# Kernel optimization log

Measured on AMD Instinct MI355X. Metric: run time of the kernel, lower is better.

The kernel has to match this reference:

```python
import jax, jax.numpy as jnp
import numpy as np

N_USERS = 100000
N_TWEETS = 100000
N_NODES = N_USERS + N_TWEETS
N_EDGES = 600000
D = 128


def lrelu(x):
    return jax.nn.leaky_relu(x, negative_slope=0.01)


def linear(x, W, b):
    # torch nn.Linear convention: W is [out, in]
    return x @ W.T + b


def rgcn_conv(x, edge_index, edge_type, weight, root, bias):
    """PyG RGCNConv with num_relations=2, aggr='mean', root weight + bias."""
    src, dst = edge_index[0], edge_index[1]
    m = x[src]  # [E, D] gathered source features
    out = x @ root + bias
    for r in range(weight.shape[0]):
        mask = (edge_type == r).astype(x.dtype)  # [E]
        s = jax.ops.segment_sum(m * mask[:, None], dst, num_segments=N_NODES)
        cnt = jax.ops.segment_sum(mask, dst, num_segments=N_NODES)
        mean = s / jnp.maximum(cnt, 1.0)[:, None]  # nodes w/o rel-r in-edges -> 0
        out = out + mean @ weight[r]
    return out


def setup_inputs() -> dict:
    key = jax.random.key(0)
    ks = jax.random.split(key, 24)

    def lin(k, out_d, in_d):
        k1, k2 = jax.random.split(k)
        s = 1.0 / np.sqrt(in_d)
        return (jax.random.uniform(k1, (out_d, in_d), jnp.float32, -s, s),
                jax.random.uniform(k2, (out_d,), jnp.float32, -s, s))

    des = jax.random.normal(ks[0], (N_USERS, 100), jnp.float32)
    tweet = jax.random.normal(ks[1], (N_TWEETS, 100), jnp.float32)
    num_prop = jax.random.normal(ks[2], (N_USERS, 6), jnp.float32)
    cat_prop = jax.random.normal(ks[3], (N_USERS, 11), jnp.float32)
    edge_index = jax.random.randint(ks[4], (2, N_EDGES), 0, N_NODES, jnp.int32)
    edge_type = jax.random.randint(ks[5], (N_EDGES,), 0, 2, jnp.int32)

    W_des, b_des = lin(ks[6], D // 2, 100)       # des -> 64
    W_num, b_num = lin(ks[7], D // 4, 6)         # num_prop -> 32
    W_cat, b_cat = lin(ks[8], D // 4, 11)        # cat_prop -> 32
    W_tw, b_tw = lin(ks[9], D, 100)              # tweet -> 128
    W_in, b_in = lin(ks[10], D, D)
    rgcn_w = jax.random.normal(ks[11], (2, D, D), jnp.float32) / np.sqrt(D)
    rgcn_root = jax.random.normal(ks[12], (D, D), jnp.float32) / np.sqrt(D)
    rgcn_bias = jnp.zeros((D,), jnp.float32)
    W_o1, b_o1 = lin(ks[13], D, D)
    W_o2, b_o2 = lin(ks[14], 2, D)

    return dict(des=des, tweet=tweet, num_prop=num_prop, cat_prop=cat_prop,
                edge_index=edge_index, edge_type=edge_type,
                W_des=W_des, b_des=b_des, W_num=W_num, b_num=b_num,
                W_cat=W_cat, b_cat=b_cat, W_tw=W_tw, b_tw=b_tw,
                W_in=W_in, b_in=b_in, rgcn_w=rgcn_w, rgcn_root=rgcn_root,
                rgcn_bias=rgcn_bias, W_o1=W_o1, b_o1=b_o1, W_o2=W_o2, b_o2=b_o2)


def reference(des, tweet, num_prop, cat_prop, edge_index, edge_type,
              W_des, b_des, W_num, b_num, W_cat, b_cat, W_tw, b_tw,
              W_in, b_in, rgcn_w, rgcn_root, rgcn_bias, W_o1, b_o1, W_o2, b_o2):
    d = lrelu(linear(des, W_des, b_des))
    n = lrelu(linear(num_prop, W_num, b_num))
    c = lrelu(linear(cat_prop, W_cat, b_cat))
    x_users = jnp.concatenate([d, n, c], axis=1)       # [N_users, 128]
    t = lrelu(linear(tweet, W_tw, b_tw))               # [N_tweets, 128]
    x = jnp.concatenate([x_users, t], axis=0)          # [N_nodes, 128]
    x = lrelu(linear(x, W_in, b_in))
    x = rgcn_conv(x, edge_index, edge_type, rgcn_w, rgcn_root, rgcn_bias)
    # dropout in eval mode = identity
    x = rgcn_conv(x, edge_index, edge_type, rgcn_w, rgcn_root, rgcn_bias)
    x = lrelu(linear(x, W_o1, b_o1))
    return linear(x, W_o2, b_o2)
```

## Files before the change

kernel.cpp:

```cpp
#include <hip/hip_runtime.h>
#include <hip/hip_bf16.h>

typedef __hip_bfloat16 bf16;

typedef __bf16 bfv8 __attribute__((ext_vector_type(8)));
typedef float f32x4 __attribute__((ext_vector_type(4)));

__device__ __forceinline__ float lrelu(float x) { return x > 0.f ? x : 0.01f * x; }

__device__ __forceinline__ float ldv(float v) { return v; }
__device__ __forceinline__ float ldv(bf16 v) { return __bfloat162float(v); }
__device__ __forceinline__ void stv(float* p, float v) { *p = v; }
__device__ __forceinline__ void stv(bf16* p, float v) { *p = __float2bfloat16(v); }

__device__ __forceinline__ float in_rd(const void* p, size_t i, int isbf) {
  return isbf ? __bfloat162float(((const bf16*)p)[i]) : ((const float*)p)[i];
}
__device__ __forceinline__ int ix_rd(const void* p, size_t i, int is64) {
  return is64 ? (int)((const long long*)p)[i] : ((const int*)p)[i];
}

struct ProbeArgs {
  const void* p[23];
  int s[23];
  int mode[23];
};

__global__ void detect_all(ProbeArgs a, int* __restrict__ flags) {
  __shared__ int sh[256];
  int b = blockIdx.x;
  const unsigned int* w = (const unsigned int*)a.p[b];
  int s = a.s[b], mode = a.mode[b];
  int t = threadIdx.x;
  int c = 0;
  if (t < s) {
    if (mode == 0) {
      unsigned int v = w[t];
      int e = (v >> 7) & 0xFF;
      c = (e >= 100 && e <= 140) ? 1 : 0;
    } else {
      c = (w[2 * t + 1] == 0u) ? 1 : 0;
    }
  }
  sh[t] = c;
  __syncthreads();
  for (int d = 128; d; d >>= 1) {
    if (t < d) sh[t] += sh[t + d];
    __syncthreads();
  }
  if (t == 0) flags[b] = (mode == 0) ? (sh[0] * 10 >= 7 * s) : (sh[0] * 10 >= 9 * s);
}

#define PW_F32 82562
#define BF_BASE 82564
#define PW_W_TOTAL (BF_BASE + 5 * 8192)
#define ENC_BASE PW_W_TOTAL
#define PW_TOTAL (ENC_BASE + 16384 + 256)
__global__ void prep_weights(const void* Win, const void* bin, const void* rw,
                             const void* root, const void* rb, const void* Wo1,
                             const void* bo1, const void* Wo2, const void* bo2,
                             const int* __restrict__ fl, float* __restrict__ pw) {
  int i = blockIdx.x * 256 + threadIdx.x;
  if (i >= PW_W_TOTAL) return;
  if (i < 16384) {
    int k = i >> 7, o = i & 127;
    pw[i] = in_rd(Win, (size_t)o * 128 + k, fl[14]);
  } else if (i < 32768) {
    int j = i - 16384;
    int k = j >> 7, o = j & 127;
    pw[i] = in_rd(Wo1, (size_t)o * 128 + k, fl[19]);
  } else if (i < 49152) {
    pw[i] = in_rd(root, i - 32768, fl[17]);
  } else if (i < 81920) {
    pw[i] = in_rd(rw, i - 49152, fl[16]);
  } else if (i < 82048) {
    pw[i] = in_rd(bin, i - 81920, fl[15]);
  } else if (i < 82176) {
    pw[i] = in_rd(rb, i - 82048, fl[18]);
  } else if (i < 82304) {
    pw[i] = in_rd(bo1, i - 82176, fl[20]);
  } else if (i < 82560) {
    pw[i] = in_rd(Wo2, i - 82304, fl[21]);
  } else if (i < PW_F32) {
    pw[i] = in_rd(bo2, i - 82560, fl[22]);
  } else if (i >= BF_BASE) {
    int j = i - BF_BASE;
    bf16* bw = (bf16*)(pw + BF_BASE);
#pragma unroll
    for (int q = 0; q < 2; q++) {
      int u = 2 * j + q;
      int m = u >> 14, r = u & 16383;
      int n = r >> 7, k = r & 127;
      float v;
      if (m == 0) v = in_rd(Win, (size_t)n * 128 + k, fl[14]);
      else if (m == 1) v = in_rd(Wo1, (size_t)n * 128 + k, fl[19]);
      else if (m == 2) v = in_rd(root, (size_t)k * 128 + n, fl[17]);
      else v = in_rd(rw, (size_t)(m - 3) * 16384 + (size_t)k * 128 + n, fl[16]);
      bw[u] = __float2bfloat16(v);
    }
  }
}

__global__ void prep_enc(const void* Wd, const void* bd, const void* Wn, const void* bn,
                         const void* Wc, const void* bc, const void* Wt, const void* bt,
                         const int* __restrict__ fl, int dDes, int dNum, int dCat, int dTw,
                         float* __restrict__ pw) {
  int i = blockIdx.x * 256 + threadIdx.x;
  bf16* e = (bf16*)(pw + ENC_BASE);
  float* bU = pw + ENC_BASE + 16384;
  float* bT = bU + 128;
  if (i < 16384) {
    int n = i >> 7, k = i & 127;
    float v = 0.f;
    if (n < 64) {
      if (k < dDes) v = in_rd(Wd, (size_t)n * dDes + k, fl[6]);
    } else if (n < 96) {
      int kk = k - dDes;
      if (kk >= 0 && kk < dNum) v = in_rd(Wn, (size_t)(n - 64) * dNum + kk, fl[8]);
    } else {
      int kk = k - dDes - dNum;
      if (kk >= 0 && kk < dCat) v = in_rd(Wc, (size_t)(n - 96) * dCat + kk, fl[10]);
    }
    e[i] = __float2bfloat16(v);
  } else if (i < 32768) {
    int j = i - 16384;
    int n = j >> 7, k = j & 127;
    float v = (k < dTw) ? in_rd(Wt, (size_t)n * dTw + k, fl[12]) : 0.f;
    e[i] = __float2bfloat16(v);
  } else if (i < 32896) {
    int j = i - 32768;
    bU[j] = (j < 64) ? in_rd(bd, j, fl[7])
                     : (j < 96) ? in_rd(bn, j - 64, fl[9]) : in_rd(bc, j - 96, fl[11]);
  } else if (i < 33024) {
    bT[i - 32896] = in_rd(bt, i - 32896, fl[13]);
  }
}

__global__ void sig_fill(float* __restrict__ p, int n, float v) {
  int i = blockIdx.x * 256 + threadIdx.x;
  if (i < n) p[i] = v;
}
__global__ void zero_ints(int* __restrict__ p, int n) {
  int i = blockIdx.x * 256 + threadIdx.x;
  if (i < n) p[i] = 0;
}

__global__ void count_edges(const void* __restrict__ ei, const void* __restrict__ et,
                            const int* __restrict__ fl, int* __restrict__ cnt, int NEr,
                            int NNr) {
  int e = blockIdx.x * 256 + threadIdx.x;
  if (e >= NEr) return;
  int d = ix_rd(ei, (size_t)NEr + e, fl[4]);
  int r = ix_rd(et, e, fl[5]) & 1;
  if ((unsigned)d >= (unsigned)NNr) return;
  atomicAdd(&cnt[r * NNr + d], 1);
}

__global__ void scan_blocks(const int* __restrict__ in, int* __restrict__ out,
                            int* __restrict__ bsum, int n) {
  __shared__ int sh[256];
  int t = threadIdx.x;
  int base = blockIdx.x * 1024 + t * 4;
  int a[4];
  int s = 0;
#pragma unroll
  for (int i = 0; i < 4; i++) {
    a[i] = (base + i < n) ? in[base + i] : 0;
    s += a[i];
  }
  sh[t] = s;
  __syncthreads();
  for (int d = 1; d < 256; d <<= 1) {
    int v = (t >= d) ? sh[t - d] : 0;
    __syncthreads();
    sh[t] += v;
    __syncthreads();
  }
  int ex = sh[t] - s;
#pragma unroll
  for (int i = 0; i < 4; i++) {
    if (base + i < n) out[base + i] = ex;
    ex += a[i];
  }
  if (t == 255 && bsum) bsum[blockIdx.x] = sh[255];
}

__global__ void scan_add_inv(int* __restrict__ off, const int* __restrict__ bsumsc,
                             const int* __restrict__ cnt, float* __restrict__ inv, int n) {
  int i = blockIdx.x * 256 + threadIdx.x;
  if (i >= n) return;
  off[i] += bsumsc[i >> 10];
  inv[i] = 1.f / fmaxf((float)cnt[i], 1.f);
}

__global__ void fill_elist(const void* __restrict__ ei, const void* __restrict__ et,
                           const int* __restrict__ fl, const int* __restrict__ off,
                           int* __restrict__ fill, int* __restrict__ elist, int NEr, int NNr) {
  int e = blockIdx.x * 256 + threadIdx.x;
  if (e >= NEr) return;
  int s = ix_rd(ei, e, fl[4]);
  int d = ix_rd(ei, (size_t)NEr + e, fl[4]);
  int r = ix_rd(et, e, fl[5]) & 1;
  if ((unsigned)d >= (unsigned)NNr || (unsigned)s >= (unsigned)NNr) return;
  int idx = r * NNr + d;
  int slot = off[idx] + atomicAdd(&fill[idx], 1);
  elist[slot] = s | ((d & 127) << 24);
}

__global__ __launch_bounds__(256) void enc_gemm(const void* __restrict__ A,
                                                const void* __restrict__ W,
                                                const void* __restrict__ B,
                                                const int* __restrict__ fl, int fa, int fw,
                                                int fb, bf16* __restrict__ x, int M, int K,
                                                int N, int row0, int col0) {
  __shared__ float Wb[128 * 102];
  __shared__ float bb[128];
  int t = threadIdx.x;
  int stride = (K & 1) ? K : K + 1;
  int fA = fl[fa];
  {
    int fW = fl[fw], fB = fl[fb];
    for (int idx = t; idx < N * K; idx += 256) {
      int j = idx / K, k = idx - j * K;
      Wb[j * stride + k] = in_rd(W, (size_t)j * K + k, fW);
    }
    if (t < N) bb[t] = in_rd(B, t, fB);
  }
  __syncthreads();
  int j = t % N;
  int r = t / N;
  int R = 256 / N;
  int iEnd = blockIdx.x * 64 + 64;
  if (iEnd > M) iEnd = M;
  const float* wrow = &Wb[j * stride];
  if (!fA) {
    const float* Af = (const float*)A;
    for (int i = blockIdx.x * 64 + r; i < iEnd; i += R) {
      const float* a = Af + (size_t)i * K;
      float acc = bb[j];
      for (int k = 0; k < K; k++) acc += a[k] * wrow[k];
      stv(&x[(size_t)(row0 + i) * 128 + col0 + j], lrelu(acc));
    }
  } else {
    const bf16* Ab = (const bf16*)A;
    for (int i = blockIdx.x * 64 + r; i < iEnd; i += R) {
      const bf16* a = Ab + (size_t)i * K;
      float acc = bb[j];
      for (int k = 0; k < K; k++) acc += __bfloat162float(a[k]) * wrow[k];
      stv(&x[(size_t)(row0 + i) * 128 + col0 + j], lrelu(acc));
    }
  }
}


__global__ __launch_bounds__(256) void enc_mfma(
    const void* __restrict__ A0, const void* __restrict__ A1, const void* __restrict__ A2,
    const int* __restrict__ fl, int fi0, int fi1, int fi2, int K0, int K1, int K2,
    const bf16* __restrict__ WbE, const float* __restrict__ biasE,
    const bf16* __restrict__ WbL, const float* __restrict__ bL, bf16* __restrict__ x,
    int M, int row0) {
  __shared__ __align__(16) bf16 Xs[16384];
  int t = threadIdx.x;
  int i0 = blockIdx.x * 128;

  {
    uint4 z = {0u, 0u, 0u, 0u};
#pragma unroll
    for (int i = 0; i < 8; i++) *(uint4*)((char*)Xs + i * 4096 + t * 16) = z;
  }
  __syncthreads();

  const void* As[3] = {A0, A1, A2};
  int Ks_[3] = {K0, K1, K2};
  int fis[3] = {fi0, fi1, fi2};
  int cb = 0;
  for (int s = 0; s < 3; s++) {
    int Ks = Ks_[s];
    if (Ks <= 0) continue;
    int isbf = fl[fis[s]];
    const void* A = As[s];
    int total = 128 * Ks;
    for (int f = t; f < total; f += 256) {
      int row = f / Ks;
      int k = f - row * Ks;
      int gr = i0 + row;
      float v = (gr < M) ? in_rd(A, (size_t)gr * Ks + k, isbf) : 0.f;
      int byte = row * 256 + (cb + k) * 2;
      *(bf16*)((char*)Xs + (byte ^ ((row & 7) << 4))) = __float2bfloat16(v);
    }
    cb += Ks;
  }
  __syncthreads();

  int wv = t >> 6, l = t & 63;
  int lr = l & 15, lg = l >> 4;
  int rbase = (wv >> 1) * 64, cbase = (wv & 1) * 64;
  int ko = lg * 8;
  f32x4 acc[4][4] = {};
#pragma unroll
  for (int ks = 0; ks < 4; ks++) {
    bfv8 bk[4];
#pragma unroll
    for (int cg = 0; cg < 4; cg++)
      bk[cg] = *(const bfv8*)&WbE[(size_t)(cbase + cg * 16 + lr) * 128 + ks * 32 + ko];
    bfv8 af[4];
#pragma unroll
    for (int rg = 0; rg < 4; rg++) {
      int mrow = rbase + rg * 16 + lr;
      int byte = mrow * 256 + (ks * 32 + ko) * 2;
      af[rg] = *(const bfv8*)((const char*)Xs + (byte ^ ((mrow & 7) << 4)));
    }
#pragma unroll
    for (int rg = 0; rg < 4; rg++)
#pragma unroll
      for (int cg = 0; cg < 4; cg++)
        acc[rg][cg] =
            __builtin_amdgcn_mfma_f32_16x16x32_bf16(af[rg], bk[cg], acc[rg][cg], 0, 0, 0);
  }
  __syncthreads();

#pragma unroll
  for (int cg = 0; cg < 4; cg++) {
    int col = cbase + cg * 16 + lr;
    float bv = biasE[col];
#pragma unroll
    for (int rg = 0; rg < 4; rg++) {
      int r0 = rbase + rg * 16 + lg * 4;
#pragma unroll
      for (int j = 0; j < 4; j++) {
        int row = r0 + j;
        int byte = row * 256 + col * 2;
        *(bf16*)((char*)Xs + (byte ^ ((row & 7) << 4))) =
            __float2bfloat16(lrelu(acc[rg][cg][j] + bv));
      }
    }
  }
  __syncthreads();

  f32x4 acc2[4][4] = {};
#pragma unroll
  for (int ks = 0; ks < 4; ks++) {
    bfv8 bk[4];
#pragma unroll
    for (int cg = 0; cg < 4; cg++)
      bk[cg] = *(const bfv8*)&WbL[(size_t)(cbase + cg * 16 + lr) * 128 + ks * 32 + ko];
    bfv8 af[4];
#pragma unroll
    for (int rg = 0; rg < 4; rg++) {
      int mrow = rbase + rg * 16 + lr;
      int byte = mrow * 256 + (ks * 32 + ko) * 2;
      af[rg] = *(const bfv8*)((const char*)Xs + (byte ^ ((mrow & 7) << 4)));
    }
#pragma unroll
    for (int rg = 0; rg < 4; rg++)
#pragma unroll
      for (int cg = 0; cg < 4; cg++)
        acc2[rg][cg] =
            __builtin_amdgcn_mfma_f32_16x16x32_bf16(af[rg], bk[cg], acc2[rg][cg], 0, 0, 0);
  }

#pragma unroll
  for (int cg = 0; cg < 4; cg++) {
    int col = cbase + cg * 16 + lr;
    float bv = bL[col];
#pragma unroll
    for (int rg = 0; rg < 4; rg++) {
      int r0 = i0 + rbase + rg * 16 + lg * 4;
#pragma unroll
      for (int j = 0; j < 4; j++) {
        int row = r0 + j;
        if (row < M)
          x[(size_t)(row0 + row) * 128 + col] = __float2bfloat16(lrelu(acc2[rg][cg][j] + bv));
      }
    }
  }
}

__global__ __launch_bounds__(256) void mfma_lin(const bf16* __restrict__ A,
                                                const bf16* __restrict__ Wb,
                                                const float* __restrict__ bias,
                                                bf16* __restrict__ Out, int M) {
  int t = threadIdx.x;
  int wv = t >> 6, l = t & 63;
  int lr = l & 15, lg = l >> 4;
  int i0 = blockIdx.x * 128;
  int rbase = (wv >> 1) * 64;
  int cbase = (wv & 1) * 64;
  int ko = lg * 8;

  size_t rowoff[4];
#pragma unroll
  for (int rg = 0; rg < 4; rg++) {
    int row = i0 + rbase + rg * 16 + lr;
    if (row > M - 1) row = M - 1;
    rowoff[rg] = (size_t)row * 128;
  }

  bfv8 bfr[4][4];
#pragma unroll
  for (int cg = 0; cg < 4; cg++)
#pragma unroll
    for (int ks = 0; ks < 4; ks++)
      bfr[cg][ks] = *(const bfv8*)&Wb[(size_t)(cbase + cg * 16 + lr) * 128 + ks * 32 + ko];

  f32x4 acc[4][4] = {};
#pragma unroll
  for (int ks = 0; ks < 4; ks++) {
    bfv8 af[4];
#pragma unroll
    for (int rg = 0; rg < 4; rg++) af[rg] = *(const bfv8*)&A[rowoff[rg] + ks * 32 + ko];
#pragma unroll
    for (int rg = 0; rg < 4; rg++)
#pragma unroll
      for (int cg = 0; cg < 4; cg++)
        acc[rg][cg] =
            __builtin_amdgcn_mfma_f32_16x16x32_bf16(af[rg], bfr[cg][ks], acc[rg][cg], 0, 0, 0);
  }

#pragma unroll
  for (int cg = 0; cg < 4; cg++) {
    int col = cbase + cg * 16 + lr;
    float bv = bias[col];
#pragma unroll
    for (int rg = 0; rg < 4; rg++) {
      int row0 = i0 + rbase + rg * 16 + lg * 4;
#pragma unroll
      for (int j = 0; j < 4; j++) {
        int row = row0 + j;
        if (row < M) Out[(size_t)row * 128 + col] = __float2bfloat16(lrelu(acc[rg][cg][j] + bv));
      }
    }
  }
}

template <bool TAIL>
__global__ __launch_bounds__(256, 4) void mfma_conv_f(
    const bf16* __restrict__ X, const int* __restrict__ off, const int* __restrict__ cnt,
    const int* __restrict__ elist, const float* __restrict__ inv,
    const bf16* __restrict__ WB, const float* __restrict__ bias, bf16* __restrict__ Out,
    const bf16* __restrict__ Wo1B, const float* __restrict__ bO1,
    const float* __restrict__ Wo2, const float* __restrict__ bo2,
    float* __restrict__ out2, int M, int NNr, int NEr) {
  __shared__ __align__(16) float At[64 * 128];
  int t = threadIdx.x;
  int wv = t >> 6, l = t & 63;
  int lr = l & 15, lg = l >> 4;
  int i0 = blockIdx.x * 32;
  int cbase = wv * 32;
  int ko = lg * 8;

  {
    int c8 = (t & 15) * 8;
    int stc[4], dgc[4];
#pragma unroll
    for (int pn = 0; pn < 4; pn++) {
      int vr = (t >> 4) + pn * 16;
      int rel = vr >> 5, m = vr & 31;
      int node = i0 + m;
      int idx = rel * NNr + node;
      bool ok = node < M;
      stc[pn] = ok ? off[idx] : 0;
      dgc[pn] = ok ? cnt[idx] : 0;
    }
    int dmax = max(max(dgc[0], dgc[1]), max(dgc[2], dgc[3]));
    float s[4][8] = {};

    auto xoff = [&](int pn, int e) -> size_t {
      int ec = e < dgc[pn] - 1 ? e : dgc[pn] - 1;
      ec = ec < 0 ? 0 : ec;
      int ei = stc[pn] + ec;
      ei = ei < NEr - 1 ? ei : NEr - 1;
      return (size_t)(elist[ei] & 0xFFFFFF) * 128 + c8;
    };

    bfv8 v0[4], v1[4];
#pragma unroll
    for (int pn = 0; pn < 4; pn++) v0[pn] = *(const bfv8*)&X[xoff(pn, 0)];
#pragma unroll
    for (int pn = 0; pn < 4; pn++) v1[pn] = *(const bfv8*)&X[xoff(pn, 1)];

    for (int e = 0; e < dmax; e++) {
      bfv8 v2[4];
#pragma unroll
      for (int pn = 0; pn < 4; pn++) v2[pn] = *(const bfv8*)&X[xoff(pn, e + 2)];
#pragma unroll
      for (int pn = 0; pn < 4; pn++) {
        float msk = e < dgc[pn] ? 1.f : 0.f;
#pragma unroll
        for (int j = 0; j < 8; j++) s[pn][j] += msk * __bfloat162float(v0[pn][j]);
      }
#pragma unroll
      for (int pn = 0; pn < 4; pn++) {
        v0[pn] = v1[pn];
        v1[pn] = v2[pn];
      }
    }
#pragma unroll
    for (int pn = 0; pn < 4; pn++) {
      int vr = (t >> 4) + pn * 16;
      int sw = (vr & 7) << 4;
      int lb = vr * 512 + c8 * 4;
      *(float4*)((char*)At + (lb ^ sw)) = make_float4(s[pn][0], s[pn][1], s[pn][2], s[pn][3]);
      *(float4*)((char*)At + ((lb + 16) ^ sw)) =
          make_float4(s[pn][4], s[pn][5], s[pn][6], s[pn][7]);
    }
  }

  size_t rowoff[2];
  float iv0[2], iv1[2];
#pragma unroll
  for (int rg = 0; rg < 2; rg++) {
    int row = i0 + rg * 16 + lr;
    int rc = row < M ? row : M - 1;
    rowoff[rg] = (size_t)rc * 128;
    iv0[rg] = row < M ? inv[row] : 0.f;
    iv1[rg] = row < M ? inv[NNr + row] : 0.f;
  }

  f32x4 acc[2][2] = {};

#pragma unroll
  for (int ks = 0; ks < 4; ks++) {
    bfv8 bk[2];
#pragma unroll
    for (int cg = 0; cg < 2; cg++)
      bk[cg] = *(const bfv8*)&WB[(size_t)(cbase + cg * 16 + lr) * 128 + ks * 32 + ko];
    bfv8 af[2];
#pragma unroll
    for (int rg = 0; rg < 2; rg++) af[rg] = *(const bfv8*)&X[rowoff[rg] + ks * 32 + ko];
#pragma unroll
    for (int rg = 0; rg < 2; rg++)
#pragma unroll
      for (int cg = 0; cg < 2; cg++)
        acc[rg][cg] =
            __builtin_amdgcn_mfma_f32_16x16x32_bf16(af[rg], bk[cg], acc[rg][cg], 0, 0, 0);
  }
  __syncthreads();

#pragma unroll
  for (int r = 0; r < 2; r++) {
    const bf16* Wb = WB + 16384 * (1 + r);
#pragma unroll
    for (int ks = 0; ks < 4; ks++) {
      bfv8 bk[2];
#pragma unroll
      for (int cg = 0; cg < 2; cg++)
        bk[cg] = *(const bfv8*)&Wb[(size_t)(cbase + cg * 16 + lr) * 128 + ks * 32 + ko];
      bfv8 af[2];
#pragma unroll
      for (int rg = 0; rg < 2; rg++) {
        int mrow = r * 32 + rg * 16 + lr;
        int lb = mrow * 512 + ks * 128 + ko * 4;
        int sw = (mrow & 7) << 4;
        float4 f0 = *(const float4*)((const char*)At + (lb ^ sw));
        float4 f1 = *(const float4*)((const char*)At + ((lb + 16) ^ sw));
        float iv = r ? iv1[rg] : iv0[rg];
        bfv8 a;
        a[0] = (__bf16)(f0.x * iv); a[1] = (__bf16)(f0.y * iv);
        a[2] = (__bf16)(f0.z * iv); a[3] = (__bf16)(f0.w * iv);
        a[4] = (__bf16)(f1.x * iv); a[5] = (__bf16)(f1.y * iv);
        a[6] = (__bf16)(f1.z * iv); a[7] = (__bf16)(f1.w * iv);
        af[rg] = a;
      }
#pragma unroll
      for (int rg = 0; rg < 2; rg++)
#pragma unroll
        for (int cg = 0; cg < 2; cg++)
          acc[rg][cg] =
              __builtin_amdgcn_mfma_f32_16x16x32_bf16(af[rg], bk[cg], acc[rg][cg], 0, 0, 0);
    }
  }

  if (!TAIL) {
#pragma unroll
    for (int cg = 0; cg < 2; cg++) {
      int col = cbase + cg * 16 + lr;
      float bv = bias[col];
#pragma unroll
      for (int rg = 0; rg < 2; rg++) {
        int row0 = i0 + rg * 16 + lg * 4;
#pragma unroll
        for (int j = 0; j < 4; j++) {
          int row = row0 + j;
          if (row < M) Out[(size_t)row * 128 + col] = __float2bfloat16(acc[rg][cg][j] + bv);
        }
      }
    }
  } else {
    __syncthreads();
#pragma unroll
    for (int cg = 0; cg < 2; cg++) {
      int col = cbase + cg * 16 + lr;
      float bv = bias[col];
#pragma unroll
      for (int rg = 0; rg < 2; rg++) {
#pragma unroll
        for (int j = 0; j < 4; j++) {
          int row32 = rg * 16 + lg * 4 + j;
          int byte = row32 * 256 + col * 2;
          *(bf16*)((char*)At + (byte ^ ((row32 & 7) << 4))) =
              __float2bfloat16(acc[rg][cg][j] + bv);
        }
      }
    }
    __syncthreads();

    f32x4 acc2[2][2] = {};
#pragma unroll
    for (int ks = 0; ks < 4; ks++) {
      bfv8 bk[2];
#pragma unroll
      for (int cg = 0; cg < 2; cg++)
        bk[cg] = *(const bfv8*)&Wo1B[(size_t)(cbase + cg * 16 + lr) * 128 + ks * 32 + ko];
      bfv8 af[2];
#pragma unroll
      for (int rg = 0; rg < 2; rg++) {
        int mrow = rg * 16 + lr;
        int byte = mrow * 256 + (ks * 32 + ko) * 2;
        af[rg] = *(const bfv8*)((const char*)At + (byte ^ ((mrow & 7) << 4)));
      }
#pragma unroll
      for (int rg = 0; rg < 2; rg++)
#pragma unroll
        for (int cg = 0; cg < 2; cg++)
          acc2[rg][cg] =
              __builtin_amdgcn_mfma_f32_16x16x32_bf16(af[rg], bk[cg], acc2[rg][cg], 0, 0, 0);
    }
#pragma unroll
    for (int cg = 0; cg < 2; cg++) {
      int col = cbase + cg * 16 + lr;
      float bv = bO1[col];
#pragma unroll
      for (int rg = 0; rg < 2; rg++) {
#pragma unroll
        for (int j = 0; j < 4; j++) {
          int row32 = rg * 16 + lg * 4 + j;
          *(bf16*)((char*)At + 8192 + row32 * 256 + col * 2) =
              __float2bfloat16(lrelu(acc2[rg][cg][j] + bv));
        }
      }
    }
    __syncthreads();

    int row = t >> 3, seg = t & 7;
    const bf16* zr = (const bf16*)((const char*)At + 8192 + row * 256 + seg * 32);
    float p0 = 0.f, p1 = 0.f;
#pragma unroll
    for (int q = 0; q < 16; q++) {
      float xv = __bfloat162float(zr[q]);
      int col = seg * 16 + q;
      p0 += xv * Wo2[col];
      p1 += xv * Wo2[128 + col];
    }
#pragma unroll
    for (int o = 4; o; o >>= 1) {
      p0 += __shfl_down(p0, o, 8);
      p1 += __shfl_down(p1, o, 8);
    }
    int grow = i0 + row;
    if (seg == 0 && grow < M) {
      out2[(size_t)grow * 2] = p0 + bo2[0];
      out2[(size_t)grow * 2 + 1] = p1 + bo2[1];
    }
  }
}

static void run_pipeline(void* const* d_in, const int* S, float* out, char* ws,
                         int NUr, int NTr, int NEr, int dDes, int dNum, int dCat, int dTw,
                         hipStream_t stream) {
  const int NNr = NUr + NTr;
  const size_t xbytes = (size_t)NNr * 128 * 2;

  bf16* xa = (bf16*)ws;
  bf16* xb = (bf16*)(ws + xbytes);
  char* p = ws + 2 * xbytes;
  int* cnt = (int*)p;      p += (size_t)2 * NNr * 4;
  int* fill = (int*)p;     p += (size_t)2 * NNr * 4;
  int* off = (int*)p;      p += (size_t)2 * NNr * 4;
  int* bsum = (int*)p;     p += 2048 * 4;
  int* bsumsc = (int*)p;   p += 2048 * 4;
  float* inv = (float*)p;  p += (size_t)2 * NNr * 4;
  int* elist = (int*)p;    p += (size_t)NEr * 4;
  float* pw = (float*)p;   p += (size_t)PW_TOTAL * 4;
  int* flags = (int*)p;

  ProbeArgs pa;
  for (int i = 0; i < 23; i++) {
    int src = (i == 22) ? 21 : i;
    pa.p[i] = d_in[src];
    if (i == 4) {
      pa.mode[i] = 1;
      pa.s[i] = NEr < 256 ? NEr : 256;
    } else if (i == 5) {
      pa.mode[i] = 1;
      int s2 = NEr / 2 < 256 ? NEr / 2 : 256;
      pa.s[i] = s2 < 1 ? 1 : s2;
    } else {
      pa.mode[i] = 0;
      int s = S[src] / 2;
      if (s > 256) s = 256;
      if (s < 1) s = 1;
      pa.s[i] = s;
    }
  }
  detect_all<<<23, 256, 0, stream>>>(pa, flags);
  prep_weights<<<(PW_W_TOTAL + 255) / 256, 256, 0, stream>>>(
      d_in[14], d_in[15], d_in[16], d_in[17], d_in[18], d_in[19], d_in[20], d_in[21],
      d_in[22], flags, pw);
  prep_enc<<<129, 256, 0, stream>>>(d_in[6], d_in[7], d_in[8], d_in[9], d_in[10], d_in[11],
                                    d_in[12], d_in[13], flags, dDes, dNum, dCat, dTw, pw);

  const float* bIn = pw + 81920;
  const float* rbp = pw + 82048;
  const float* bO1 = pw + 82176;
  const float* Wo2p = pw + 82304;
  const float* bo2p = pw + 82560;
  const bf16* WinB = (const bf16*)(pw + BF_BASE);
  const bf16* Wo1B = (const bf16*)(pw + BF_BASE + 8192);
  const bf16* ConvB = (const bf16*)(pw + BF_BASE + 16384);
  const bf16* EncU = (const bf16*)(pw + ENC_BASE);
  const bf16* EncT = (const bf16*)(pw + ENC_BASE + 8192);
  const float* bU = pw + ENC_BASE + 16384;
  const float* bT = bU + 128;

  const void* ei = d_in[4];
  const void* et = d_in[5];
  const int nb1 = (2 * NNr + 1023) / 1024;

  zero_ints<<<(4 * NNr + 255) / 256, 256, 0, stream>>>(cnt, 4 * NNr);
  zero_ints<<<16, 256, 0, stream>>>(bsum, 4096);
  count_edges<<<(NEr + 255) / 256, 256, 0, stream>>>(ei, et, flags, cnt, NEr, NNr);
  scan_blocks<<<nb1, 256, 0, stream>>>(cnt, off, bsum, 2 * NNr);
  scan_blocks<<<1, 256, 0, stream>>>(bsum, bsumsc, nullptr, nb1);
  scan_add_inv<<<(2 * NNr + 255) / 256, 256, 0, stream>>>(off, bsumsc, cnt, inv, 2 * NNr);
  fill_elist<<<(NEr + 255) / 256, 256, 0, stream>>>(ei, et, flags, off, fill, elist, NEr, NNr);

  if (dDes + dNum + dCat <= 128 && dTw <= 128) {
    enc_mfma<<<(NUr + 127) / 128, 256, 0, stream>>>(d_in[0], d_in[2], d_in[3], flags, 0, 2, 3,
                                                    dDes, dNum, dCat, EncU, bU, WinB, bIn, xb,
                                                    NUr, 0);
    enc_mfma<<<(NTr + 127) / 128, 256, 0, stream>>>(d_in[1], nullptr, nullptr, flags, 1, 1, 1,
                                                    dTw, 0, 0, EncT, bT, WinB, bIn, xb, NTr,
                                                    NUr);
  } else {
    enc_gemm<<<(NUr + 63) / 64, 256, 0, stream>>>(d_in[0], d_in[6], d_in[7], flags, 0, 6, 7,
                                                  xa, NUr, dDes, 64, 0, 0);
    enc_gemm<<<(NUr + 63) / 64, 256, 0, stream>>>(d_in[2], d_in[8], d_in[9], flags, 2, 8, 9,
                                                  xa, NUr, dNum, 32, 0, 64);
    enc_gemm<<<(NUr + 63) / 64, 256, 0, stream>>>(d_in[3], d_in[10], d_in[11], flags, 3, 10,
                                                  11, xa, NUr, dCat, 32, 0, 96);
    enc_gemm<<<(NTr + 63) / 64, 256, 0, stream>>>(d_in[1], d_in[12], d_in[13], flags, 1, 12,
                                                  13, xa, NTr, dTw, 128, NUr, 0);
    mfma_lin<<<(NNr + 127) / 128, 256, 0, stream>>>(xa, WinB, bIn, xb, NNr);
  }

  const int mt32 = (NNr + 31) / 32;
  mfma_conv_f<false><<<mt32, 256, 0, stream>>>(xb, off, cnt, elist, inv, ConvB, rbp, xa,
                                               nullptr, nullptr, nullptr, nullptr, nullptr,
                                               NNr, NNr, NEr);
  mfma_conv_f<true><<<mt32, 256, 0, stream>>>(xa, off, cnt, elist, inv, ConvB, rbp, nullptr,
                                              Wo1B, bO1, Wo2p, bo2p, out, NNr, NNr, NEr);
}

extern "C" void kernel_launch(void* const* d_in, const int* in_sizes, int n_in,
                              void* d_out, int out_size, void* d_ws, size_t ws_size,
                              hipStream_t stream) {
  float* out = (float*)d_out;
  char* ws = (char*)d_ws;

  auto signal = [&](int k) {
    sig_fill<<<(out_size + 255) / 256, 256, 0, stream>>>(out, out_size, (float)(200 + k));
  };

  if (n_in != 23) { signal(1); return; }
  const int* S = in_sizes;
  if (S[7] != 64 || S[9] != 32 || S[11] != 32 || S[13] != 128) { signal(2); return; }
  if (S[15] != 128) { signal(3); return; }
  if (S[6] % 64 || S[8] % 32 || S[10] % 32 || S[12] % 128) { signal(4); return; }
  int dDes = S[6] / 64, dNum = S[8] / 32, dCat = S[10] / 32, dTw = S[12] / 128;
  if (dDes <= 0 || dTw <= 0 || S[0] % dDes || S[1] % dTw) { signal(5); return; }
  if (dDes > 101 || dNum > 101 || dCat > 101 || dTw > 101) { signal(4); return; }
  int NUr = S[0] / dDes, NTr = S[1] / dTw, NNr = NUr + NTr, NEr = S[5];
  if (S[2] != NUr * dNum || S[3] != NUr * dCat) { signal(5); return; }
  if (S[4] != 2 * NEr || NEr < 1024) { signal(6); return; }
  if (NNr >= (1 << 24)) { signal(6); return; }
  if (S[14] != 16384 || S[16] != 32768 || S[17] != 16384 || S[18] != 128 ||
      S[19] != 16384 || S[20] != 128 || S[21] != 256 || S[22] != 2) { signal(7); return; }
  if (out_size != NNr * 2) { signal(8); return; }

  const size_t smallBytes = (size_t)4 * ((size_t)2 * NNr * 4) + 2 * 2048 * 4 +
                            (size_t)NEr * 4 + (size_t)PW_TOTAL * 4 + 512;
  const size_t need = 2 * (size_t)NNr * 128 * 2 + smallBytes;

  if (ws_size >= need) {
    run_pipeline(d_in, S, out, ws, NUr, NTr, NEr, dDes, dNum, dCat, dTw, stream);
  } else {
    signal(9);
  }
}
```

Before: 520.6 us.

## Shrink conv tiles to 16 nodes and stage edge lists in LDS

The fused RGCN conv kernel now processes 16 destination nodes per block instead of 32. Each thread gathers two relation slots instead of four, and the LDS accumulator buffer is halved. Each block first copies its contiguous CSR edge-list range into shared memory, falling back to global reads past a 1024-entry cap. Occupancy hint is raised to 6 blocks per CU. The aim is more parallelism and shorter per-thread dependency chains in the latency-bound gather, at the cost of twice as many blocks reloading the weight fragments and an extra barrier.

```diff
diff --git a/kernel.cpp b/kernel.cpp
--- a/kernel.cpp
+++ b/kernel.cpp
@@ -433,71 +433,94 @@
   }
 }
 
+#define ELCAP 1024
 template <bool TAIL>
-__global__ __launch_bounds__(256, 4) void mfma_conv_f(
+__global__ __launch_bounds__(256, 6) void mfma_conv_f(
     const bf16* __restrict__ X, const int* __restrict__ off, const int* __restrict__ cnt,
     const int* __restrict__ elist, const float* __restrict__ inv,
     const bf16* __restrict__ WB, const float* __restrict__ bias, bf16* __restrict__ Out,
     const bf16* __restrict__ Wo1B, const float* __restrict__ bO1,
     const float* __restrict__ Wo2, const float* __restrict__ bo2,
     float* __restrict__ out2, int M, int NNr, int NEr) {
-  __shared__ __align__(16) float At[64 * 128];
+  __shared__ __align__(16) float At[32 * 128];
+  __shared__ int eLs[ELCAP];
   int t = threadIdx.x;
   int wv = t >> 6, l = t & 63;
   int lr = l & 15, lg = l >> 4;
-  int i0 = blockIdx.x * 32;
+  int i0 = blockIdx.x * 16;
   int cbase = wv * 32;
   int ko = lg * 8;
 
+  int iend = (i0 + 16 < M) ? i0 + 16 : M;
+  int e0a = off[i0];
+  int n0 = off[iend - 1] + cnt[iend - 1] - e0a;
+  int e0b = off[NNr + i0];
+  int n1 = off[NNr + iend - 1] + cnt[NNr + iend - 1] - e0b;
+  int staged = n0 + n1 < ELCAP ? n0 + n1 : ELCAP;
+
+  for (int k = t; k < staged; k += 256)
+    eLs[k] = (k < n0) ? elist[e0a + k] : elist[e0b + (k - n0)];
+
+  int grp = t >> 4;
+  int c8 = (t & 15) * 8;
+  int node = i0 + grp;
+  bool ok = node < M;
+  int stc[2], dgc[2], lbase[2];
   {
-    int c8 = (t & 15) * 8;
-    int stc[4], dgc[4];
-#pragma unroll
-    for (int pn = 0; pn < 4; pn++) {
-      int vr = (t >> 4) + pn * 16;
-      int rel = vr >> 5, m = vr & 31;
-      int node = i0 + m;
-      int idx = rel * NNr + node;
-      bool ok = node < M;
-      stc[pn] = ok ? off[idx] : 0;
-      dgc[pn] = ok ? cnt[idx] : 0;
-    }
-    int dmax = max(max(dgc[0], dgc[1]), max(dgc[2], dgc[3]));
-    float s[4][8] = {};
-
-    auto xoff = [&](int pn, int e) -> size_t {
+    int idx0 = node, idx1 = NNr + node;
+    stc[0] = ok ? off[idx0] : 0;
+    dgc[0] = ok ? cnt[idx0] : 0;
+    stc[1] = ok ? off[idx1] : 0;
+    dgc[1] = ok ? cnt[idx1] : 0;
+    lbase[0] = stc[0] - e0a;
+    lbase[1] = n0 + (stc[1] - e0b);
+  }
+  __syncthreads();
+
+  {
+    int dmax = dgc[0] > dgc[1] ? dgc[0] : dgc[1];
+    float s[2][8] = {};
+
+    auto srcof = [&](int pn, int e) -> size_t {
       int ec = e < dgc[pn] - 1 ? e : dgc[pn] - 1;
       ec = ec < 0 ? 0 : ec;
-      int ei = stc[pn] + ec;
-      ei = ei < NEr - 1 ? ei : NEr - 1;
-      return (size_t)(elist[ei] & 0xFFFFFF) * 128 + c8;
+      int lidx = lbase[pn] + ec;
+      int w;
+      if (lidx < staged) {
+        w = eLs[lidx];
+      } else {
+        int g = stc[pn] + ec;
+        g = g < NEr - 1 ? g : NEr - 1;
+        w = elist[g];
+      }
+      return (size_t)(w & 0xFFFFFF) * 128 + c8;
     };
 
-    bfv8 v0[4], v1[4];
-#pragma unroll
-    for (int pn = 0; pn < 4; pn++) v0[pn] = *(const bfv8*)&X[xoff(pn, 0)];
-#pragma unroll
-    for (int pn = 0; pn < 4; pn++) v1[pn] = *(const bfv8*)&X[xoff(pn, 1)];
+    bfv8 v0[2], v1[2];
+#pragma unroll
+    for (int pn = 0; pn < 2; pn++) v0[pn] = *(const bfv8*)&X[srcof(pn, 0)];
+#pragma unroll
+    for (int pn = 0; pn < 2; pn++) v1[pn] = *(const bfv8*)&X[srcof(pn, 1)];
 
     for (int e = 0; e < dmax; e++) {
-      bfv8 v2[4];
-#pragma unroll
-      for (int pn = 0; pn < 4; pn++) v2[pn] = *(const bfv8*)&X[xoff(pn, e + 2)];
-#pragma unroll
-      for (int pn = 0; pn < 4; pn++) {
+      bfv8 v2[2];
+#pragma unroll
+      for (int pn = 0; pn < 2; pn++) v2[pn] = *(const bfv8*)&X[srcof(pn, e + 2)];
+#pragma unroll
+      for (int pn = 0; pn < 2; pn++) {
         float msk = e < dgc[pn] ? 1.f : 0.f;
 #pragma unroll
         for (int j = 0; j < 8; j++) s[pn][j] += msk * __bfloat162float(v0[pn][j]);
       }
 #pragma unroll
-      for (int pn = 0; pn < 4; pn++) {
+      for (int pn = 0; pn < 2; pn++) {
         v0[pn] = v1[pn];
         v1[pn] = v2[pn];
       }
     }
 #pragma unroll
-    for (int pn = 0; pn < 4; pn++) {
-      int vr = (t >> 4) + pn * 16;
+    for (int pn = 0; pn < 2; pn++) {
+      int vr = pn * 16 + grp;
       int sw = (vr & 7) << 4;
       int lb = vr * 512 + c8 * 4;
       *(float4*)((char*)At + (lb ^ sw)) = make_float4(s[pn][0], s[pn][1], s[pn][2], s[pn][3]);
@@ -506,18 +529,17 @@
     }
   }
 
-  size_t rowoff[2];
-  float iv0[2], iv1[2];
-#pragma unroll
-  for (int rg = 0; rg < 2; rg++) {
-    int row = i0 + rg * 16 + lr;
+  size_t rowoff;
+  float iv0, iv1;
+  {
+    int row = i0 + lr;
     int rc = row < M ? row : M - 1;
-    rowoff[rg] = (size_t)rc * 128;
-    iv0[rg] = row < M ? inv[row] : 0.f;
-    iv1[rg] = row < M ? inv[NNr + row] : 0.f;
-  }
-
-  f32x4 acc[2][2] = {};
+    rowoff = (size_t)rc * 128;
+    iv0 = row < M ? inv[row] : 0.f;
+    iv1 = row < M ? inv[NNr + row] : 0.f;
+  }
+
+  f32x4 acc[2] = {};
 
 #pragma unroll
   for (int ks = 0; ks < 4; ks++) {
@@ -525,49 +547,36 @@
 #pragma unroll
     for (int cg = 0; cg < 2; cg++)
       bk[cg] = *(const bfv8*)&WB[(size_t)(cbase + cg * 16 + lr) * 128 + ks * 32 + ko];
-    bfv8 af[2];
-#pragma unroll
-    for (int rg = 0; rg < 2; rg++) af[rg] = *(const bfv8*)&X[rowoff[rg] + ks * 32 + ko];
-#pragma unroll
-    for (int rg = 0; rg < 2; rg++)
-#pragma unroll
-      for (int cg = 0; cg < 2; cg++)
-        acc[rg][cg] =
-            __builtin_amdgcn_mfma_f32_16x16x32_bf16(af[rg], bk[cg], acc[rg][cg], 0, 0, 0);
+    bfv8 af = *(const bfv8*)&X[rowoff + ks * 32 + ko];
+#pragma unroll
+    for (int cg = 0; cg < 2; cg++)
+      acc[cg] = __builtin_amdgcn_mfma_f32_16x16x32_bf16(af, bk[cg], acc[cg], 0, 0, 0);
   }
   __syncthreads();
 
 #pragma unroll
   for (int r = 0; r < 2; r++) {
     const bf16* Wb = WB + 16384 * (1 + r);
+    float iv = r ? iv1 : iv0;
 #pragma unroll
     for (int ks = 0; ks < 4; ks++) {
       bfv8 bk[2];
 #pragma unroll
       for (int cg = 0; cg < 2; cg++)
         bk[cg] = *(const bfv8*)&Wb[(size_t)(cbase + cg * 16 + lr) * 128 + ks * 32 + ko];
-      bfv8 af[2];
-#pragma unroll
-      for (int rg = 0; rg < 2; rg++) {
-        int mrow = r * 32 + rg * 16 + lr;
-        int lb = mrow * 512 + ks * 128 + ko * 4;
-        int sw = (mrow & 7) << 4;
-        float4 f0 = *(const float4*)((const char*)At + (lb ^ sw));
-        float4 f1 = *(const float4*)((const char*)At + ((lb + 16) ^ sw));
-        float iv = r ? iv1[rg] : iv0[rg];
-        bfv8 a;
-        a[0] = (__bf16)(f0.x * iv); a[1] = (__bf16)(f0.y * iv);
-        a[2] = (__bf16)(f0.z * iv); a[3] = (__bf16)(f0.w * iv);
-        a[4] = (__bf16)(f1.x * iv); a[5] = (__bf16)(f1.y * iv);
-        a[6] = (__bf16)(f1.z * iv); a[7] = (__bf16)(f1.w * iv);
-        af[rg] = a;
-      }
-#pragma unroll
-      for (int rg = 0; rg < 2; rg++)
-#pragma unroll
-        for (int cg = 0; cg < 2; cg++)
-          acc[rg][cg] =
-              __builtin_amdgcn_mfma_f32_16x16x32_bf16(af[rg], bk[cg], acc[rg][cg], 0, 0, 0);
+      int mrow = r * 16 + lr;
+      int lb = mrow * 512 + ks * 128 + ko * 4;
+      int sw = (mrow & 7) << 4;
+      float4 f0 = *(const float4*)((const char*)At + (lb ^ sw));
+      float4 f1 = *(const float4*)((const char*)At + ((lb + 16) ^ sw));
+      bfv8 a;
+      a[0] = (__bf16)(f0.x * iv); a[1] = (__bf16)(f0.y * iv);
+      a[2] = (__bf16)(f0.z * iv); a[3] = (__bf16)(f0.w * iv);
+      a[4] = (__bf16)(f1.x * iv); a[5] = (__bf16)(f1.y * iv);
+      a[6] = (__bf16)(f1.z * iv); a[7] = (__bf16)(f1.w * iv);
+#pragma unroll
+      for (int cg = 0; cg < 2; cg++)
+        acc[cg] = __builtin_amdgcn_mfma_f32_16x16x32_bf16(a, bk[cg], acc[cg], 0, 0, 0);
     }
   }
 
@@ -577,13 +586,9 @@
       int col = cbase + cg * 16 + lr;
       float bv = bias[col];
 #pragma unroll
-      for (int rg = 0; rg < 2; rg++) {
-        int row0 = i0 + rg * 16 + lg * 4;
-#pragma unroll
-        for (int j = 0; j < 4; j++) {
-          int row = row0 + j;
-          if (row < M) Out[(size_t)row * 128 + col] = __float2bfloat16(acc[rg][cg][j] + bv);
-        }
+      for (int j = 0; j < 4; j++) {
+        int row = i0 + lg * 4 + j;
+        if (row < M) Out[(size_t)row * 128 + col] = __float2bfloat16(acc[cg][j] + bv);
       }
     }
   } else {
@@ -593,69 +598,54 @@
       int col = cbase + cg * 16 + lr;
       float bv = bias[col];
 #pragma unroll
-      for (int rg = 0; rg < 2; rg++) {
-#pragma unroll
-        for (int j = 0; j < 4; j++) {
-          int row32 = rg * 16 + lg * 4 + j;
-          int byte = row32 * 256 + col * 2;
-          *(bf16*)((char*)At + (byte ^ ((row32 & 7) << 4))) =
-              __float2bfloat16(acc[rg][cg][j] + bv);
-        }
+      for (int j = 0; j < 4; j++) {
+        int r16 = lg * 4 + j;
+        int byte = r16 * 256 + col * 2;
+        *(bf16*)((char*)At + (byte ^ ((r16 & 7) << 4))) = __float2bfloat16(acc[cg][j] + bv);
       }
     }
     __syncthreads();
 
-    f32x4 acc2[2][2] = {};
+    f32x4 acc2[2] = {};
 #pragma unroll
     for (int ks = 0; ks < 4; ks++) {
       bfv8 bk[2];
 #pragma unroll
       for (int cg = 0; cg < 2; cg++)
         bk[cg] = *(const bfv8*)&Wo1B[(size_t)(cbase + cg * 16 + lr) * 128 + ks * 32 + ko];
-      bfv8 af[2];
-#pragma unroll
-      for (int rg = 0; rg < 2; rg++) {
-        int mrow = rg * 16 + lr;
-        int byte = mrow * 256 + (ks * 32 + ko) * 2;
-        af[rg] = *(const bfv8*)((const char*)At + (byte ^ ((mrow & 7) << 4)));
-      }
-#pragma unroll
-      for (int rg = 0; rg < 2; rg++)
-#pragma unroll
-        for (int cg = 0; cg < 2; cg++)
-          acc2[rg][cg] =
-              __builtin_amdgcn_mfma_f32_16x16x32_bf16(af[rg], bk[cg], acc2[rg][cg], 0, 0, 0);
+      int byte = lr * 256 + (ks * 32 + ko) * 2;
+      bfv8 af = *(const bfv8*)((const char*)At + (byte ^ ((lr & 7) << 4)));
+#pragma unroll
+      for (int cg = 0; cg < 2; cg++)
+        acc2[cg] = __builtin_amdgcn_mfma_f32_16x16x32_bf16(af, bk[cg], acc2[cg], 0, 0, 0);
     }
 #pragma unroll
     for (int cg = 0; cg < 2; cg++) {
       int col = cbase + cg * 16 + lr;
       float bv = bO1[col];
 #pragma unroll
-      for (int rg = 0; rg < 2; rg++) {
-#pragma unroll
-        for (int j = 0; j < 4; j++) {
-          int row32 = rg * 16 + lg * 4 + j;
-          *(bf16*)((char*)At + 8192 + row32 * 256 + col * 2) =
-              __float2bfloat16(lrelu(acc2[rg][cg][j] + bv));
-        }
+      for (int j = 0; j < 4; j++) {
+        int r16 = lg * 4 + j;
+        *(bf16*)((char*)At + 8192 + r16 * 256 + col * 2) =
+            __float2bfloat16(lrelu(acc2[cg][j] + bv));
       }
     }
     __syncthreads();
 
-    int row = t >> 3, seg = t & 7;
-    const bf16* zr = (const bf16*)((const char*)At + 8192 + row * 256 + seg * 32);
+    int row = t >> 4, seg = t & 15;
+    const bf16* zr = (const bf16*)((const char*)At + 8192 + row * 256 + seg * 16);
     float p0 = 0.f, p1 = 0.f;
 #pragma unroll
-    for (int q = 0; q < 16; q++) {
+    for (int q = 0; q < 8; q++) {
       float xv = __bfloat162float(zr[q]);
-      int col = seg * 16 + q;
+      int col = seg * 8 + q;
       p0 += xv * Wo2[col];
       p1 += xv * Wo2[128 + col];
     }
 #pragma unroll
-    for (int o = 4; o; o >>= 1) {
-      p0 += __shfl_down(p0, o, 8);
-      p1 += __shfl_down(p1, o, 8);
+    for (int o = 8; o; o >>= 1) {
+      p0 += __shfl_down(p0, o, 16);
+      p1 += __shfl_down(p1, o, 16);
     }
     int grow = i0 + row;
     if (seg == 0 && grow < M) {
@@ -754,11 +744,11 @@
     mfma_lin<<<(NNr + 127) / 128, 256, 0, stream>>>(xa, WinB, bIn, xb, NNr);
   }
 
-  const int mt32 = (NNr + 31) / 32;
-  mfma_conv_f<false><<<mt32, 256, 0, stream>>>(xb, off, cnt, elist, inv, ConvB, rbp, xa,
+  const int mt16 = (NNr + 15) / 16;
+  mfma_conv_f<false><<<mt16, 256, 0, stream>>>(xb, off, cnt, elist, inv, ConvB, rbp, xa,
                                                nullptr, nullptr, nullptr, nullptr, nullptr,
                                                NNr, NNr, NEr);
-  mfma_conv_f<true><<<mt32, 256, 0, stream>>>(xa, off, cnt, elist, inv, ConvB, rbp, nullptr,
+  mfma_conv_f<true><<<mt16, 256, 0, stream>>>(xa, off, cnt, elist, inv, ConvB, rbp, nullptr,
                                               Wo1B, bO1, Wo2p, bo2p, out, NNr, NNr, NEr);
 }
 
```

Result: slower. 648.0 us (+24.5%).

## Stage block edge lists in LDS and gather two edges per iteration

Applied to the files above, without the earlier changes.

Each block first copies its contiguous range of edge-list entries for both relations into a shared-memory buffer, so the per-edge index lookups in the gather loop read LDS instead of global memory, with a fallback to global when the cap is exceeded. The gather loop is changed from a two-deep software prefetch to unrolled pairs of edges, issuing eight feature loads per iteration. Launch bounds drop to 3 blocks per CU to make room for the extra LDS and registers. The cost is an extra staging pass and a barrier per block, and lower occupancy that may hide less gather latency.

```diff
diff --git a/kernel.cpp b/kernel.cpp
--- a/kernel.cpp
+++ b/kernel.cpp
@@ -433,8 +433,9 @@
   }
 }
 
+#define ELCAP 2048
 template <bool TAIL>
-__global__ __launch_bounds__(256, 4) void mfma_conv_f(
+__global__ __launch_bounds__(256, 3) void mfma_conv_f(
     const bf16* __restrict__ X, const int* __restrict__ off, const int* __restrict__ cnt,
     const int* __restrict__ elist, const float* __restrict__ inv,
     const bf16* __restrict__ WB, const float* __restrict__ bias, bf16* __restrict__ Out,
@@ -442,6 +443,7 @@
     const float* __restrict__ Wo2, const float* __restrict__ bo2,
     float* __restrict__ out2, int M, int NNr, int NEr) {
   __shared__ __align__(16) float At[64 * 128];
+  __shared__ int eLs[ELCAP];
   int t = threadIdx.x;
   int wv = t >> 6, l = t & 63;
   int lr = l & 15, lg = l >> 4;
@@ -449,61 +451,77 @@
   int cbase = wv * 32;
   int ko = lg * 8;
 
+  int iend = (i0 + 32 < M) ? i0 + 32 : M;
+  int e0a = off[i0];
+  int n0 = off[iend - 1] + cnt[iend - 1] - e0a;
+  int e0b = off[NNr + i0];
+  int n1 = off[NNr + iend - 1] + cnt[NNr + iend - 1] - e0b;
+  int staged = n0 + n1 < ELCAP ? n0 + n1 : ELCAP;
+
+  for (int k = t; k < staged; k += 256)
+    eLs[k] = (k < n0) ? elist[e0a + k] : elist[e0b + (k - n0)];
+
+  int grp = t >> 4;
+  int c8 = (t & 15) * 8;
+  int stc[4], dgc[4], lbase[4];
+#pragma unroll
+  for (int pn = 0; pn < 4; pn++) {
+    int vr = grp + pn * 16;
+    int rel = vr >> 5, m = vr & 31;
+    int node = i0 + m;
+    bool ok = node < M;
+    int idx = rel * NNr + node;
+    int so = ok ? off[idx] : 0;
+    stc[pn] = so;
+    dgc[pn] = ok ? cnt[idx] : 0;
+    lbase[pn] = ok ? (rel ? n0 + (so - e0b) : so - e0a) : 0;
+  }
+  __syncthreads();
+
+  float s[4][8] = {};
   {
-    int c8 = (t & 15) * 8;
-    int stc[4], dgc[4];
-#pragma unroll
-    for (int pn = 0; pn < 4; pn++) {
-      int vr = (t >> 4) + pn * 16;
-      int rel = vr >> 5, m = vr & 31;
-      int node = i0 + m;
-      int idx = rel * NNr + node;
-      bool ok = node < M;
-      stc[pn] = ok ? off[idx] : 0;
-      dgc[pn] = ok ? cnt[idx] : 0;
-    }
     int dmax = max(max(dgc[0], dgc[1]), max(dgc[2], dgc[3]));
-    float s[4][8] = {};
-
-    auto xoff = [&](int pn, int e) -> size_t {
+
+    auto eword = [&](int pn, int e) -> unsigned {
       int ec = e < dgc[pn] - 1 ? e : dgc[pn] - 1;
       ec = ec < 0 ? 0 : ec;
-      int ei = stc[pn] + ec;
-      ei = ei < NEr - 1 ? ei : NEr - 1;
-      return (size_t)(elist[ei] & 0xFFFFFF) * 128 + c8;
+      int li = lbase[pn] + ec;
+      if (li < staged) return (unsigned)eLs[li];
+      int g = stc[pn] + ec;
+      g = g < NEr - 1 ? g : NEr - 1;
+      return (unsigned)elist[g];
     };
 
-    bfv8 v0[4], v1[4];
-#pragma unroll
-    for (int pn = 0; pn < 4; pn++) v0[pn] = *(const bfv8*)&X[xoff(pn, 0)];
-#pragma unroll
-    for (int pn = 0; pn < 4; pn++) v1[pn] = *(const bfv8*)&X[xoff(pn, 1)];
-
-    for (int e = 0; e < dmax; e++) {
-      bfv8 v2[4];
-#pragma unroll
-      for (int pn = 0; pn < 4; pn++) v2[pn] = *(const bfv8*)&X[xoff(pn, e + 2)];
+    for (int e0 = 0; e0 < dmax; e0 += 2) {
+      unsigned wbuf[8];
 #pragma unroll
       for (int pn = 0; pn < 4; pn++) {
-        float msk = e < dgc[pn] ? 1.f : 0.f;
-#pragma unroll
-        for (int j = 0; j < 8; j++) s[pn][j] += msk * __bfloat162float(v0[pn][j]);
-      }
+        wbuf[2 * pn] = eword(pn, e0);
+        wbuf[2 * pn + 1] = eword(pn, e0 + 1);
+      }
+      bfv8 v[8];
+#pragma unroll
+      for (int q = 0; q < 8; q++)
+        v[q] = *(const bfv8*)&X[(size_t)(wbuf[q] & 0xFFFFFF) * 128 + c8];
 #pragma unroll
       for (int pn = 0; pn < 4; pn++) {
-        v0[pn] = v1[pn];
-        v1[pn] = v2[pn];
-      }
-    }
-#pragma unroll
-    for (int pn = 0; pn < 4; pn++) {
-      int vr = (t >> 4) + pn * 16;
-      int sw = (vr & 7) << 4;
-      int lb = vr * 512 + c8 * 4;
-      *(float4*)((char*)At + (lb ^ sw)) = make_float4(s[pn][0], s[pn][1], s[pn][2], s[pn][3]);
-      *(float4*)((char*)At + ((lb + 16) ^ sw)) =
-          make_float4(s[pn][4], s[pn][5], s[pn][6], s[pn][7]);
-    }
+        float m0 = e0 < dgc[pn] ? 1.f : 0.f;
+        float m1 = e0 + 1 < dgc[pn] ? 1.f : 0.f;
+#pragma unroll
+        for (int j = 0; j < 8; j++)
+          s[pn][j] +=
+              m0 * __bfloat162float(v[2 * pn][j]) + m1 * __bfloat162float(v[2 * pn + 1][j]);
+      }
+    }
+  }
+#pragma unroll
+  for (int pn = 0; pn < 4; pn++) {
+    int vr = grp + pn * 16;
+    int sw = (vr & 7) << 4;
+    int lb = vr * 512 + c8 * 4;
+    *(float4*)((char*)At + (lb ^ sw)) = make_float4(s[pn][0], s[pn][1], s[pn][2], s[pn][3]);
+    *(float4*)((char*)At + ((lb + 16) ^ sw)) =
+        make_float4(s[pn][4], s[pn][5], s[pn][6], s[pn][7]);
   }
 
   size_t rowoff[2];
```

Result: slower. 540.4 us (+3.8%).
